# Performance work log

Measured on AMD Instinct MI355X. Metric: run time of the kernel, lower is better.

The kernel has to match this reference:

```python
import jax, jax.numpy as jnp
import numpy as np

LR = 0.01            # learning_rate
PC = 0.001           # pred_clipping
WC = 5.0             # weight_clipping
_LO = float(np.log(PC / (1.0 - PC)))   # logit(pred_clipping)
_HI = -_LO                              # logit(1 - pred_clipping)


def setup_inputs() -> dict:
    B, S, I, CTX, M, C = 64, 1023, 1024, 784, 4, 1  # S = size-1 (bias row), C = num_classes->1
    key = jax.random.key(0)
    k = jax.random.split(key, 6)
    logit = jax.random.normal(k[0], (B, I, C), jnp.float32)
    context = jax.random.normal(k[1], (B, CTX), jnp.float32)
    target = jax.random.uniform(k[2], (B, C), dtype=jnp.float32)
    cm = jax.random.normal(k[3], (C, S, M, CTX), jnp.float32)
    cm = cm / jnp.linalg.norm(cm, axis=-1, keepdims=True)          # unit-norm context maps
    cb = jax.random.normal(k[4], (C, S, M, 1), jnp.float32)        # context bias
    weights = jnp.full((C, S, 2 ** M, I), 1.0 / I, jnp.float32)    # per-context weight table
    bias = jax.random.uniform(k[5], (1, 1, C), jnp.float32, _LO, _HI)
    return {"logit": logit, "context": context, "target": target,
            "context_maps": cm, "context_bias": cb, "weights": weights, "bias": bias}


def reference(logit, context, target, context_maps, context_bias, weights, bias):
    C, S, M, _ = context_maps.shape
    B = context.shape[0]
    # halfspace hashing of the context -> per-(class, neuron, sample) weight-table index
    dist = jnp.einsum('csmk,bk->csmb', context_maps, context)      # [C,S,M,B]
    bits = (dist > context_bias).astype(jnp.int32)
    conv = (2 ** jnp.arange(M, dtype=jnp.int32))[:, None]          # [M,1]
    idx = jnp.sum(bits * conv, axis=-2)                            # [C,S,B] in [0, 2^M)
    ci = jnp.arange(C)[:, None, None]
    si = jnp.arange(S)[None, :, None]
    sel = weights[ci, si, idx]                                     # gather -> [C,S,B,I]
    # batched dot product (torch code does full matmul + diagonal; this is the same math)
    out = jnp.clip(jnp.einsum('csbi,bic->csb', sel, logit), _LO, _HI)
    out_bsc = out.transpose(2, 1, 0)                               # [B,S,C]
    # online weight update (target branch): gather-compute-scatter
    diff = jax.nn.sigmoid(out_bsc) - target[:, None, :]            # [B,S,C]
    upd = LR * diff[..., None] * logit.transpose(0, 2, 1)[:, None, :, :]  # [B,S,C,I]
    new_sel = jnp.clip(sel - upd.transpose(2, 1, 0, 3), -WC, WC)   # [C,S,B,I]
    new_weights = weights.at[ci, si, idx].set(new_sel)             # scatter
    # prepend constant bias neuron
    out_logits = jnp.concatenate([jnp.broadcast_to(bias, (B, 1, C)), out_bsc], axis=1)  # [B,S+1,C]
    return out_logits, new_weights
```

## Files before the change

kernel.cpp:

```cpp
#include <hip/hip_runtime.h>
#include <math.h>

typedef unsigned long long u64;
typedef __attribute__((ext_vector_type(8))) short bf16x8;
typedef __attribute__((ext_vector_type(4))) float f32x4;

#define S_DIM 1023
#define B_DIM 64
#define I_DIM 1024
#define CTX_DIM 784
#define CTX4 196
#define NWROWS 16
#define HROWS 8

#define LR_C 0.01f
#define WC_C 5.0f
#define LO_C (-6.906754778648554f)
#define HI_C ( 6.906754778648554f)

__device__ __forceinline__ float dot4(float4 a, float4 b) {
    return a.x * b.x + a.y * b.y + a.z * b.z + a.w * b.w;
}

__device__ __forceinline__ float4 upd4(float4 w, float4 a, float c) {
    float4 r;
    r.x = fminf(fmaxf(w.x - c * a.x, -WC_C), WC_C);
    r.y = fminf(fmaxf(w.y - c * a.y, -WC_C), WC_C);
    r.z = fminf(fmaxf(w.z - c * a.z, -WC_C), WC_C);
    r.w = fminf(fmaxf(w.w - c * a.w, -WC_C), WC_C);
    return r;
}

__device__ __forceinline__ short f2bf(float f) {
    union { float f; unsigned u; } cv; cv.f = f;
    unsigned r = cv.u + 0x7fffu + ((cv.u >> 16) & 1u);
    return (short)(r >> 16);
}

__device__ __forceinline__ float bf2f(short h) {
    union { unsigned u; float f; } cv;
    cv.u = ((unsigned)(unsigned short)h) << 16;
    return cv.f;
}

__global__ __launch_bounds__(256) void prep_pack_kernel(
    const float* __restrict__ context,
    const float* __restrict__ bias,
    const float* __restrict__ logit,
    float4* __restrict__ ctxT4,
    short* __restrict__ pack_b,
    float* __restrict__ out_logits)
{
    const int blk = blockIdx.x;
    const int t = threadIdx.x;
    if (blk < 49) {
        int g = blk * 256 + t;
        int k4 = g >> 6;
        int b  = g & 63;
        ctxT4[g] = *(const float4*)(context + (size_t)b * CTX_DIM + k4 * 4);
        if (g < B_DIM) out_logits[(size_t)g * (S_DIM + 1)] = bias[0];
    } else {
        int g = (blk - 49) * 256 + t;
        int l  = g & 63;
        int kb = (g >> 6) & 31;
        int nt = g >> 11;
        int b  = nt * 16 + (l & 15);
        int i0 = kb * 32 + (l >> 4) * 8;
        const float* src = logit + (size_t)b * I_DIM + i0;
        bf16x8 v;
        #pragma unroll
        for (int j = 0; j < 8; ++j) v[j] = f2bf(src[j]);
        *(bf16x8*)(pack_b + (size_t)g * 8) = v;
    }
}

__global__ __launch_bounds__(256) void gln_idx_kernel(
    const float* __restrict__ cm,
    const float* __restrict__ cb,
    const float4* __restrict__ ctxT4,
    u64* __restrict__ mask_g)
{
    __shared__ float red[4][4][64];
    __shared__ int   bits[4][64];
    __shared__ float cb_lds[4];

    const int s = blockIdx.x;
    const int t = threadIdx.x;
    if (t < 4) cb_lds[t] = cb[s * 4 + t];

    const int b = t & 63;
    const int q = __builtin_amdgcn_readfirstlane(t >> 6);
    const float4* cmr = (const float4*)(cm + (size_t)s * 4 * CTX_DIM);

    float a0 = 0.f, a1 = 0.f, a2 = 0.f, a3 = 0.f;
    const int k0 = q * 49;
    #pragma unroll 7
    for (int kk = 0; kk < 49; ++kk) {
        int k4 = k0 + kk;
        float4 c4 = ctxT4[k4 * 64 + b];
        a0 += dot4(cmr[k4], c4);
        a1 += dot4(cmr[CTX4 + k4], c4);
        a2 += dot4(cmr[2 * CTX4 + k4], c4);
        a3 += dot4(cmr[3 * CTX4 + k4], c4);
    }
    red[q][0][b] = a0;
    red[q][1][b] = a1;
    red[q][2][b] = a2;
    red[q][3][b] = a3;
    __syncthreads();

    {
        int m = t >> 6, bb = t & 63;
        float sum = red[0][m][bb] + red[1][m][bb] + red[2][m][bb] + red[3][m][bb];
        bits[m][bb] = (sum > cb_lds[m]) ? 1 : 0;
    }
    __syncthreads();

    if (t < B_DIM) {
        int v = bits[0][t] + 2 * bits[1][t] + 4 * bits[2][t] + 8 * bits[3][t];
        u64 my = 0;
        #pragma unroll
        for (int kk = 0; kk < NWROWS; ++kk) {
            u64 mk = __ballot(v == kk);
            if (t == kk) my = mk;
        }
        if (t < NWROWS) mask_g[s * NWROWS + t] = my;
    }
}

__global__ __launch_bounds__(256, 8) void gln_body_kernel(
    const float* __restrict__ logit,
    const float* __restrict__ target,
    const float* __restrict__ weights,
    const u64*   __restrict__ mask_g,
    const short* __restrict__ pack_b,
    float* __restrict__ out_logits,
    float* __restrict__ new_weights)
{
    __shared__ short Abf[HROWS * I_DIM];
    __shared__ u64   mask_lds[HROWS];
    __shared__ int   lastb_lds[HROWS];
    __shared__ float coef_lds[HROWS];

    const int blk  = blockIdx.x;
    const int s    = blk >> 1;
    const int half = blk & 1;
    const int t  = threadIdx.x;
    const int wv = t >> 6;
    const int l  = t & 63;

    if (t < HROWS) {
        u64 m = mask_g[s * NWROWS + half * HROWS + t];
        mask_lds[t]  = m;
        lastb_lds[t] = m ? (63 - __clzll(m)) : -1;
    }

    const float4* W4 = (const float4*)(weights
                     + (size_t)s * (NWROWS * I_DIM) + (size_t)half * (HROWS * I_DIM));
    #pragma unroll
    for (int j = 0; j < HROWS; ++j) {
        float4 w = W4[t + j * 256];
        int slot = j * 128 + ((t >> 1) ^ j);
        short4 v;
        v.x = f2bf(w.x); v.y = f2bf(w.y); v.z = f2bf(w.z); v.w = f2bf(w.w);
        *(short4*)(Abf + slot * 8 + (t & 1) * 4) = v;
    }
    __syncthreads();

    const int row_local = l & 7;
    const int q2  = l >> 4;
    const int base_slot = row_local * 128;
    const bf16x8* Bb = (const bf16x8*)pack_b + (size_t)wv * 2048 + l;
    f32x4 acc = {0.f, 0.f, 0.f, 0.f};
    #pragma unroll 8
    for (int kb = 0; kb < 32; ++kb) {
        bf16x8 af = *(const bf16x8*)(Abf + 8 * (base_slot + ((kb * 4 + q2) ^ row_local)));
        bf16x8 bfr = Bb[(size_t)kb * 64];
        acc = __builtin_amdgcn_mfma_f32_16x16x32_bf16(af, bfr, acc, 0, 0, 0);
    }

    const int col = wv * 16 + (l & 15);
    if (q2 < 2) {
        #pragma unroll
        for (int j = 0; j < 4; ++j) {
            int r = q2 * 4 + j;
            u64 m = mask_lds[r];
            if ((m >> col) & 1) {
                float o = fminf(fmaxf(acc[j], LO_C), HI_C);
                out_logits[(size_t)col * (S_DIM + 1) + s + 1] = o;
                if (col == lastb_lds[r])
                    coef_lds[r] = LR_C * (1.0f / (1.0f + expf(-o)) - target[col]);
            }
        }
    }
    __syncthreads();

    float4* D4 = (float4*)(new_weights
               + (size_t)s * (NWROWS * I_DIM) + (size_t)half * (HROWS * I_DIM));
    const float4* L4 = (const float4*)logit;
    #pragma unroll 4
    for (int r = 0; r < HROWS; ++r) {
        const int lb = lastb_lds[r];
        int slot = r * 128 + ((t >> 1) ^ r);
        short4 v = *(const short4*)(Abf + slot * 8 + (t & 1) * 4);
        float4 w;
        w.x = bf2f(v.x); w.y = bf2f(v.y); w.z = bf2f(v.z); w.w = bf2f(v.w);
        float4 o;
        if (lb < 0) {
            o = w;
        } else {
            o = upd4(w, L4[lb * 256 + t], coef_lds[r]);
        }
        D4[r * 256 + t] = o;
    }
}

extern "C" void kernel_launch(void* const* d_in, const int* in_sizes, int n_in,
                              void* d_out, int out_size, void* d_ws, size_t ws_size,
                              hipStream_t stream) {
    const float* logit   = (const float*)d_in[0];
    const float* context = (const float*)d_in[1];
    const float* target  = (const float*)d_in[2];
    const float* cm      = (const float*)d_in[3];
    const float* cb      = (const float*)d_in[4];
    const float* weights = (const float*)d_in[5];
    const float* bias    = (const float*)d_in[6];

    float* out_logits  = (float*)d_out;
    float* new_weights = out_logits + (size_t)B_DIM * (S_DIM + 1);

    char* ws = (char*)d_ws;
    float4* ctxT4  = (float4*)ws;    ws += (size_t)CTX4 * B_DIM * 16;
    short*  packb  = (short*)ws;     ws += (size_t)4 * 32 * 64 * 8 * 2;
    u64*    mask_g = (u64*)ws;

    prep_pack_kernel<<<81, 256, 0, stream>>>(context, bias, logit, ctxT4, packb, out_logits);
    gln_idx_kernel<<<S_DIM, 256, 0, stream>>>(cm, cb, ctxT4, mask_g);
    gln_body_kernel<<<S_DIM * 2, 256, 0, stream>>>(logit, target, weights, mask_g, packb,
                                                   out_logits, new_weights);
}
```

Measured before the change: 53.47 us.

## Double-buffer weight tiles in persistent body kernel and add control weight copy

```diff
diff --git a/kernel.cpp b/kernel.cpp
--- a/kernel.cpp
+++ b/kernel.cpp
@@ -12,6 +12,8 @@
 #define CTX4 196
 #define NWROWS 16
 #define HROWS 8
+#define NHALF (S_DIM * 2)
+#define G_S 4
 
 #define LR_C 0.01f
 #define WC_C 5.0f
@@ -41,6 +43,17 @@
     union { unsigned u; float f; } cv;
     cv.u = ((unsigned)(unsigned short)h) << 16;
     return cv.f;
+}
+
+__global__ __launch_bounds__(256) void ctrl_copy_kernel(
+    const float4* __restrict__ src, float4* __restrict__ dst)
+{
+    const int g = blockIdx.x * 256 + threadIdx.x;
+    #pragma unroll
+    for (int k = 0; k < 4; ++k) {
+        int i = g + k * 524288;
+        dst[i] = src[i];
+    }
 }
 
 __global__ __launch_bounds__(256) void prep_pack_kernel(
@@ -128,7 +141,7 @@
     }
 }
 
-__global__ __launch_bounds__(256, 8) void gln_body_kernel(
+__global__ __launch_bounds__(256, 4) void gln_pipe_kernel(
     const float* __restrict__ logit,
     const float* __restrict__ target,
     const float* __restrict__ weights,
@@ -137,33 +150,37 @@
     float* __restrict__ out_logits,
     float* __restrict__ new_weights)
 {
-    __shared__ short Abf[HROWS * I_DIM];
-    __shared__ u64   mask_lds[HROWS];
-    __shared__ int   lastb_lds[HROWS];
-    __shared__ float coef_lds[HROWS];
-
-    const int blk  = blockIdx.x;
-    const int s    = blk >> 1;
-    const int half = blk & 1;
+    __shared__ short Abf[2][HROWS * I_DIM];
+    __shared__ u64   mask_lds[2][HROWS];
+    __shared__ int   lastb_lds[2][HROWS];
+    __shared__ float coef_lds[2][HROWS];
+
     const int t  = threadIdx.x;
     const int wv = t >> 6;
     const int l  = t & 63;
-
-    if (t < HROWS) {
-        u64 m = mask_g[s * NWROWS + half * HROWS + t];
-        mask_lds[t]  = m;
-        lastb_lds[t] = m ? (63 - __clzll(m)) : -1;
-    }
-
-    const float4* W4 = (const float4*)(weights
-                     + (size_t)s * (NWROWS * I_DIM) + (size_t)half * (HROWS * I_DIM));
-    #pragma unroll
-    for (int j = 0; j < HROWS; ++j) {
-        float4 w = W4[t + j * 256];
-        int slot = j * 128 + ((t >> 1) ^ j);
-        short4 v;
-        v.x = f2bf(w.x); v.y = f2bf(w.y); v.z = f2bf(w.z); v.w = f2bf(w.w);
-        *(short4*)(Abf + slot * 8 + (t & 1) * 4) = v;
+    const int h0 = blockIdx.x * G_S;
+
+    const float4* L4 = (const float4*)logit;
+
+    {
+        const int h = h0;
+        const float4* W4 = (const float4*)weights + (size_t)h * (HROWS * 256);
+        float4 ld[8];
+        #pragma unroll
+        for (int j = 0; j < HROWS; ++j) ld[j] = W4[t + j * 256];
+        if (t < HROWS) {
+            u64 m = mask_g[(size_t)h * HROWS + t];
+            mask_lds[0][t]  = m;
+            lastb_lds[0][t] = m ? (63 - __clzll(m)) : -1;
+        }
+        #pragma unroll
+        for (int j = 0; j < HROWS; ++j) {
+            int slot = j * 128 + ((t >> 1) ^ j);
+            short4 v;
+            v.x = f2bf(ld[j].x); v.y = f2bf(ld[j].y);
+            v.z = f2bf(ld[j].z); v.w = f2bf(ld[j].w);
+            *(short4*)(&Abf[0][0] + slot * 8 + (t & 1) * 4) = v;
+        }
     }
     __syncthreads();
 
@@ -171,47 +188,84 @@
     const int q2  = l >> 4;
     const int base_slot = row_local * 128;
     const bf16x8* Bb = (const bf16x8*)pack_b + (size_t)wv * 2048 + l;
-    f32x4 acc = {0.f, 0.f, 0.f, 0.f};
-    #pragma unroll 8
-    for (int kb = 0; kb < 32; ++kb) {
-        bf16x8 af = *(const bf16x8*)(Abf + 8 * (base_slot + ((kb * 4 + q2) ^ row_local)));
-        bf16x8 bfr = Bb[(size_t)kb * 64];
-        acc = __builtin_amdgcn_mfma_f32_16x16x32_bf16(af, bfr, acc, 0, 0, 0);
-    }
-
     const int col = wv * 16 + (l & 15);
-    if (q2 < 2) {
-        #pragma unroll
-        for (int j = 0; j < 4; ++j) {
-            int r = q2 * 4 + j;
-            u64 m = mask_lds[r];
-            if ((m >> col) & 1) {
-                float o = fminf(fmaxf(acc[j], LO_C), HI_C);
-                out_logits[(size_t)col * (S_DIM + 1) + s + 1] = o;
-                if (col == lastb_lds[r])
-                    coef_lds[r] = LR_C * (1.0f / (1.0f + expf(-o)) - target[col]);
-            }
-        }
-    }
-    __syncthreads();
-
-    float4* D4 = (float4*)(new_weights
-               + (size_t)s * (NWROWS * I_DIM) + (size_t)half * (HROWS * I_DIM));
-    const float4* L4 = (const float4*)logit;
-    #pragma unroll 4
-    for (int r = 0; r < HROWS; ++r) {
-        const int lb = lastb_lds[r];
-        int slot = r * 128 + ((t >> 1) ^ r);
-        short4 v = *(const short4*)(Abf + slot * 8 + (t & 1) * 4);
-        float4 w;
-        w.x = bf2f(v.x); w.y = bf2f(v.y); w.z = bf2f(v.z); w.w = bf2f(v.w);
-        float4 o;
-        if (lb < 0) {
-            o = w;
-        } else {
-            o = upd4(w, L4[lb * 256 + t], coef_lds[r]);
-        }
-        D4[r * 256 + t] = o;
+
+    for (int g = 0; g < G_S; ++g) {
+        const int h = h0 + g;
+        const bool valid = (h < NHALF);
+        const int cur = g & 1;
+        const int s = h >> 1;
+
+        if (valid) {
+            f32x4 acc = {0.f, 0.f, 0.f, 0.f};
+            const short* A = &Abf[cur][0];
+            #pragma unroll 8
+            for (int kb = 0; kb < 32; ++kb) {
+                bf16x8 af = *(const bf16x8*)(A + 8 * (base_slot + ((kb * 4 + q2) ^ row_local)));
+                bf16x8 bfr = Bb[(size_t)kb * 64];
+                acc = __builtin_amdgcn_mfma_f32_16x16x32_bf16(af, bfr, acc, 0, 0, 0);
+            }
+            if (q2 < 2) {
+                #pragma unroll
+                for (int j = 0; j < 4; ++j) {
+                    int r = q2 * 4 + j;
+                    u64 m = mask_lds[cur][r];
+                    if ((m >> col) & 1) {
+                        float o = fminf(fmaxf(acc[j], LO_C), HI_C);
+                        out_logits[(size_t)col * (S_DIM + 1) + s + 1] = o;
+                        if (col == lastb_lds[cur][r])
+                            coef_lds[cur][r] = LR_C * (1.0f / (1.0f + expf(-o)) - target[col]);
+                    }
+                }
+            }
+        }
+        __syncthreads();
+
+        const int hn = h + 1;
+        const bool nvalid = (g + 1 < G_S) && (hn < NHALF);
+        float4 ld[8];
+        if (nvalid) {
+            const float4* W4n = (const float4*)weights + (size_t)hn * (HROWS * 256);
+            #pragma unroll
+            for (int j = 0; j < HROWS; ++j) ld[j] = W4n[t + j * 256];
+            if (t < HROWS) {
+                u64 m = mask_g[(size_t)hn * HROWS + t];
+                mask_lds[cur ^ 1][t]  = m;
+                lastb_lds[cur ^ 1][t] = m ? (63 - __clzll(m)) : -1;
+            }
+        }
+
+        if (valid) {
+            float4* D4 = (float4*)new_weights + (size_t)h * (HROWS * 256);
+            const short* A = &Abf[cur][0];
+            #pragma unroll 4
+            for (int r = 0; r < HROWS; ++r) {
+                const int lb = lastb_lds[cur][r];
+                int slot = r * 128 + ((t >> 1) ^ r);
+                short4 v = *(const short4*)(A + slot * 8 + (t & 1) * 4);
+                float4 w;
+                w.x = bf2f(v.x); w.y = bf2f(v.y); w.z = bf2f(v.z); w.w = bf2f(v.w);
+                float4 o;
+                if (lb < 0) {
+                    o = w;
+                } else {
+                    o = upd4(w, L4[lb * 256 + t], coef_lds[cur][r]);
+                }
+                D4[r * 256 + t] = o;
+            }
+        }
+
+        if (nvalid) {
+            #pragma unroll
+            for (int j = 0; j < HROWS; ++j) {
+                int slot = j * 128 + ((t >> 1) ^ j);
+                short4 v;
+                v.x = f2bf(ld[j].x); v.y = f2bf(ld[j].y);
+                v.z = f2bf(ld[j].z); v.w = f2bf(ld[j].w);
+                *(short4*)(&Abf[cur ^ 1][0] + slot * 8 + (t & 1) * 4) = v;
+            }
+        }
+        __syncthreads();
     }
 }
 
@@ -234,8 +288,10 @@
     short*  packb  = (short*)ws;     ws += (size_t)4 * 32 * 64 * 8 * 2;
     u64*    mask_g = (u64*)ws;
 
+    ctrl_copy_kernel<<<2048, 256, 0, stream>>>((const float4*)weights,
+                                               (float4*)new_weights);
     prep_pack_kernel<<<81, 256, 0, stream>>>(context, bias, logit, ctxT4, packb, out_logits);
     gln_idx_kernel<<<S_DIM, 256, 0, stream>>>(cm, cb, ctxT4, mask_g);
-    gln_body_kernel<<<S_DIM * 2, 256, 0, stream>>>(logit, target, weights, mask_g, packb,
-                                                   out_logits, new_weights);
-}
+    gln_pipe_kernel<<<(NHALF + G_S - 1) / G_S, 256, 0, stream>>>(
+        logit, target, weights, mask_g, packb, out_logits, new_weights);
+}
```

Result: slower. 68.10 us (+27.4%).

## Stage fp32 weights into LDS via direct global-to-LDS loads, convert to bf16 at MFMA

Applied to the files above, without the earlier changes.

```diff
diff --git a/kernel.cpp b/kernel.cpp
--- a/kernel.cpp
+++ b/kernel.cpp
@@ -12,6 +12,7 @@
 #define CTX4 196
 #define NWROWS 16
 #define HROWS 8
+#define ROWF 1028
 
 #define LR_C 0.01f
 #define WC_C 5.0f
@@ -35,12 +36,6 @@
     union { float f; unsigned u; } cv; cv.f = f;
     unsigned r = cv.u + 0x7fffu + ((cv.u >> 16) & 1u);
     return (short)(r >> 16);
-}
-
-__device__ __forceinline__ float bf2f(short h) {
-    union { unsigned u; float f; } cv;
-    cv.u = ((unsigned)(unsigned short)h) << 16;
-    return cv.f;
 }
 
 __global__ __launch_bounds__(256) void prep_pack_kernel(
@@ -128,7 +123,7 @@
     }
 }
 
-__global__ __launch_bounds__(256, 8) void gln_body_kernel(
+__global__ __launch_bounds__(256, 4) void gln_body_kernel(
     const float* __restrict__ logit,
     const float* __restrict__ target,
     const float* __restrict__ weights,
@@ -137,7 +132,7 @@
     float* __restrict__ out_logits,
     float* __restrict__ new_weights)
 {
-    __shared__ short Abf[HROWS * I_DIM];
+    __shared__ __align__(16) float Wlds[HROWS * ROWF];
     __shared__ u64   mask_lds[HROWS];
     __shared__ int   lastb_lds[HROWS];
     __shared__ float coef_lds[HROWS];
@@ -149,69 +144,71 @@
     const int wv = t >> 6;
     const int l  = t & 63;
 
+    const float* Wbase = weights + (size_t)s * (NWROWS * I_DIM)
+                       + (size_t)half * (HROWS * I_DIM);
+    #pragma unroll
+    for (int j = 0; j < HROWS; ++j) {
+        const float* g = Wbase + j * I_DIM + wv * 256 + l * 4;
+        float* p = &Wlds[j * ROWF + wv * 256];
+        __builtin_amdgcn_global_load_lds(
+            (const __attribute__((address_space(1))) void*)g,
+            (__attribute__((address_space(3))) void*)p, 16, 0, 0);
+    }
+
     if (t < HROWS) {
         u64 m = mask_g[s * NWROWS + half * HROWS + t];
         mask_lds[t]  = m;
         lastb_lds[t] = m ? (63 - __clzll(m)) : -1;
     }
-
-    const float4* W4 = (const float4*)(weights
-                     + (size_t)s * (NWROWS * I_DIM) + (size_t)half * (HROWS * I_DIM));
-    #pragma unroll
-    for (int j = 0; j < HROWS; ++j) {
-        float4 w = W4[t + j * 256];
-        int slot = j * 128 + ((t >> 1) ^ j);
-        short4 v;
-        v.x = f2bf(w.x); v.y = f2bf(w.y); v.z = f2bf(w.z); v.w = f2bf(w.w);
-        *(short4*)(Abf + slot * 8 + (t & 1) * 4) = v;
-    }
-    __syncthreads();
-
-    const int row_local = l & 7;
-    const int q2  = l >> 4;
-    const int base_slot = row_local * 128;
+    __syncthreads();
+
+    const int r  = l & 7;
+    const int co = (l >> 4) * 8;
+    const float* Arow = &Wlds[r * ROWF + co];
     const bf16x8* Bb = (const bf16x8*)pack_b + (size_t)wv * 2048 + l;
     f32x4 acc = {0.f, 0.f, 0.f, 0.f};
     #pragma unroll 8
     for (int kb = 0; kb < 32; ++kb) {
-        bf16x8 af = *(const bf16x8*)(Abf + 8 * (base_slot + ((kb * 4 + q2) ^ row_local)));
+        float4 x = *(const float4*)(Arow + kb * 32);
+        float4 y = *(const float4*)(Arow + kb * 32 + 4);
+        bf16x8 af;
+        af[0] = f2bf(x.x); af[1] = f2bf(x.y); af[2] = f2bf(x.z); af[3] = f2bf(x.w);
+        af[4] = f2bf(y.x); af[5] = f2bf(y.y); af[6] = f2bf(y.z); af[7] = f2bf(y.w);
         bf16x8 bfr = Bb[(size_t)kb * 64];
         acc = __builtin_amdgcn_mfma_f32_16x16x32_bf16(af, bfr, acc, 0, 0, 0);
     }
 
     const int col = wv * 16 + (l & 15);
+    const int q2  = l >> 4;
     if (q2 < 2) {
         #pragma unroll
         for (int j = 0; j < 4; ++j) {
-            int r = q2 * 4 + j;
-            u64 m = mask_lds[r];
+            int rr = q2 * 4 + j;
+            u64 m = mask_lds[rr];
             if ((m >> col) & 1) {
                 float o = fminf(fmaxf(acc[j], LO_C), HI_C);
                 out_logits[(size_t)col * (S_DIM + 1) + s + 1] = o;
-                if (col == lastb_lds[r])
-                    coef_lds[r] = LR_C * (1.0f / (1.0f + expf(-o)) - target[col]);
+                if (col == lastb_lds[rr])
+                    coef_lds[rr] = LR_C * (1.0f / (1.0f + expf(-o)) - target[col]);
             }
         }
     }
     __syncthreads();
 
-    float4* D4 = (float4*)(new_weights
-               + (size_t)s * (NWROWS * I_DIM) + (size_t)half * (HROWS * I_DIM));
+    float4* D4 = (float4*)(new_weights + (size_t)s * (NWROWS * I_DIM)
+               + (size_t)half * (HROWS * I_DIM));
     const float4* L4 = (const float4*)logit;
     #pragma unroll 4
-    for (int r = 0; r < HROWS; ++r) {
-        const int lb = lastb_lds[r];
-        int slot = r * 128 + ((t >> 1) ^ r);
-        short4 v = *(const short4*)(Abf + slot * 8 + (t & 1) * 4);
-        float4 w;
-        w.x = bf2f(v.x); w.y = bf2f(v.y); w.z = bf2f(v.z); w.w = bf2f(v.w);
+    for (int rr = 0; rr < HROWS; ++rr) {
+        const int lb = lastb_lds[rr];
+        float4 w = *(const float4*)&Wlds[rr * ROWF + t * 4];
         float4 o;
         if (lb < 0) {
             o = w;
         } else {
-            o = upd4(w, L4[lb * 256 + t], coef_lds[r]);
+            o = upd4(w, L4[lb * 256 + t], coef_lds[rr]);
         }
-        D4[r * 256 + t] = o;
+        D4[rr * 256 + t] = o;
     }
 }
 
```

Measured after the change: 67.44 us. 1.26x slower.
